# Kernel tuning notes

Hardware: AMD Instinct MI355X
Metric: run time of the kernel (lower is better)

Reference implementation:

```python
import jax, jax.numpy as jnp
import numpy as np

B = 2048          # batch
F = 32            # input feature size
H = 512           # lstm hidden size
BN = 64           # autoencoder bottleneck
OUT = 8           # final dense output size
SEQ_LEN = 128
LOOK_AHEAD = 32
RS, RE = 0, 8     # replace_start, replace_end (RE-RS == OUT)


def setup_inputs() -> dict:
    key = jax.random.key(0)
    ks = jax.random.split(key, 16)
    s = lambda k, shape: (jax.random.normal(k, shape, jnp.float32) * 0.05)
    return {
        'x': jax.random.normal(ks[0], (B, SEQ_LEN + LOOK_AHEAD, F), jnp.float32),
        # layer-0 LSTMCell (input F)
        'Wih0': s(ks[1], (F, 4 * H)), 'Whh0': s(ks[2], (H, 4 * H)),
        'bih0': s(ks[3], (4 * H,)),   'bhh0': s(ks[4], (4 * H,)),
        # layer-1 LSTMCell (input H)
        'Wih1': s(ks[5], (H, 4 * H)), 'Whh1': s(ks[6], (H, 4 * H)),
        'bih1': s(ks[7], (4 * H,)),   'bhh1': s(ks[8], (4 * H,)),
        # discretizing autoencoder: 2H -> BN -> 2H (shared across layers)
        'We': s(ks[9], (2 * H, BN)),  'be': s(ks[10], (BN,)),
        'Wd': s(ks[11], (BN, 2 * H)), 'bd': s(ks[12], (2 * H,)),
        # final dense H -> OUT
        'Wf': s(ks[13], (H, OUT)),    'bf': s(ks[14], (OUT,)),
    }


def _lstm_cell(x, h, c, Wih, Whh, bih, bhh):
    # torch.nn.LSTMCell gate order: i, f, g, o
    g = x @ Wih + bih + h @ Whh + bhh          # [B, 4H]
    i, f, gg, o = jnp.split(g, 4, axis=1)
    i, f, o = jax.nn.sigmoid(i), jax.nn.sigmoid(f), jax.nn.sigmoid(o)
    c2 = f * c + i * jnp.tanh(gg)
    return o * jnp.tanh(c2), c2


def _ae(z, We, be, Wd, bd):
    # bottleneck with straight-through rounding (discretization)
    b = jnp.tanh(z @ We + be)
    q = b + jax.lax.stop_gradient(jnp.round(b) - b)
    return q @ Wd + bd


def _layers_fwd(x_t, st, p):
    h0, c0, h1, c1 = st
    hc = _ae(jnp.concatenate([h0, c0], axis=1), p['We'], p['be'], p['Wd'], p['bd'])
    h0, c0 = jnp.split(hc, 2, axis=1)
    h0, c0 = _lstm_cell(x_t, h0, c0, p['Wih0'], p['Whh0'], p['bih0'], p['bhh0'])
    # dropout layer between stacked layers is identity in eval mode
    hc = _ae(jnp.concatenate([h1, c1], axis=1), p['We'], p['be'], p['Wd'], p['bd'])
    h1, c1 = jnp.split(hc, 2, axis=1)
    h1, c1 = _lstm_cell(h0, h1, c1, p['Wih1'], p['Whh1'], p['bih1'], p['bhh1'])
    return (h0, c0, h1, c1)


def reference(x, Wih0, Whh0, bih0, bhh0, Wih1, Whh1, bih1, bhh1,
              We, be, Wd, bd, Wf, bf):
    p = dict(Wih0=Wih0, Whh0=Whh0, bih0=bih0, bhh0=bhh0,
             Wih1=Wih1, Whh1=Whh1, bih1=bih1, bhh1=bhh1,
             We=We, be=be, Wd=Wd, bd=bd)
    bsz = x.shape[0]
    z = jnp.zeros((bsz, H), x.dtype)
    st = (z, z, z, z)

    # warm-up phase over seq_len observed steps
    def step1(st, x_t):
        return _layers_fwd(x_t, st, p), None
    st, _ = jax.lax.scan(step1, st, jnp.swapaxes(x[:, :SEQ_LEN], 0, 1))
    out0 = st[2] @ Wf + bf  # final dense on top-layer h

    def step2(carry, x_t):
        st, out = carry
        x_t = x_t.at[:, RS:RE].set(out)
        st = _layers_fwd(x_t, st, p)
        out = st[2] @ Wf + bf
        return (st, out), out
    (_, _), outs = jax.lax.scan(step2, (st, out0),
                                jnp.swapaxes(x[:, SEQ_LEN:SEQ_LEN + LOOK_AHEAD], 0, 1))

    # [B, 1 + look_ahead, OUT]
    return jnp.concatenate([out0[:, None, :], jnp.swapaxes(outs, 0, 1)], axis=1)
```

## Files before the change

kernel.cpp:

```cpp
#include <hip/hip_runtime.h>
#include <hip/hip_bf16.h>
#include <math.h>

#define NB    2048
#define FIN   32
#define HH    512
#define G4    2048
#define BNE   64
#define OUTD  8
#define SEQL  128
#define LOOK  32
#define TOT   (SEQL + LOOK)
#define TB    8
#define NTHR  1024

__device__ __forceinline__ float sigf(float v) { return 1.0f / (1.0f + expf(-v)); }

#define MAC2(S, HS)                                    \
  {                                                    \
    a[S].x = fmaf(w.x, (HS), a[S].x);                  \
    a[S].y = fmaf(w.y, (HS), a[S].y);                  \
  }
#define MAC2x8()                                       \
  {                                                    \
    MAC2(0, hA.x); MAC2(1, hA.y); MAC2(2, hA.z); MAC2(3, hA.w); \
    MAC2(4, hB.x); MAC2(5, hB.y); MAC2(6, hB.z); MAC2(7, hB.w); \
  }

__global__ __launch_bounds__(NTHR)
void fused_rnn(const float* __restrict__ x,
               const float* __restrict__ Wih0, const float* __restrict__ Whh0,
               const float* __restrict__ bih0, const float* __restrict__ bhh0,
               const float* __restrict__ Wih1, const float* __restrict__ Whh1,
               const float* __restrict__ bih1, const float* __restrict__ bhh1,
               const float* __restrict__ We,   const float* __restrict__ be,
               const float* __restrict__ Wd,   const float* __restrict__ bd,
               const float* __restrict__ Wf,   const float* __restrict__ bf,
               float* __restrict__ out)
{
  __shared__ float sh0[HH][TB], sc0[HH][TB], sh1[HH][TB], sc1[HH][TB];
  __shared__ float sg[TB][G4];
  __shared__ float sq[2][BNE][TB];
  __shared__ float sx[FIN][TB];
  __shared__ float sout[TB][OUTD];

  const int t  = threadIdx.x;
  const int b0 = blockIdx.x * TB;

  for (int i = t; i < HH * TB; i += NTHR) {
    (&sh0[0][0])[i] = 0.f; (&sc0[0][0])[i] = 0.f;
    (&sh1[0][0])[i] = 0.f; (&sc1[0][0])[i] = 0.f;
  }

  const float2 bb0 = make_float2(bih0[2*t]   + bhh0[2*t],
                                 bih0[2*t+1] + bhh0[2*t+1]);
  const float2 bb1 = make_float2(bih1[2*t]   + bhh1[2*t],
                                 bih1[2*t+1] + bhh1[2*t+1]);

  const double Athr = 0.5493061443340549;

  for (int step = 0; step < TOT; ++step) {
    __syncthreads();

    {
      const int ae = t >> 9, s = (t >> 6) & 7, n = t & 63;
      const float* Sh = ae ? &sh1[0][0] : &sh0[0][0];
      const float* Sc = ae ? &sc1[0][0] : &sc0[0][0];
      double a0 = (double)be[n];
      const float* we0 = We + n;
#pragma unroll 4
      for (int k = 0; k < HH; k++)
        a0 = fma((double)Sh[k * TB + s], (double)we0[(size_t)k * BNE], a0);
      const float* we1 = We + (size_t)HH * BNE + n;
#pragma unroll 4
      for (int k = 0; k < HH; k++)
        a0 = fma((double)Sc[k * TB + s], (double)we1[(size_t)k * BNE], a0);
      sq[ae][n][s] = (a0 > Athr) ? 1.f : ((a0 < -Athr) ? -1.f : 0.f);
    }
    __syncthreads();

    {
      float aq0[TB], aq1[TB];
      const float bdv = bd[t];
#pragma unroll
      for (int s = 0; s < TB; s++) { aq0[s] = bdv; aq1[s] = bdv; }
      const float* wd = Wd + t;
#pragma unroll 2
      for (int j = 0; j < BNE; j++) {
        const float w = wd[(size_t)j * (2 * HH)];
        const float4 qA0 = *(const float4*)&sq[0][j][0];
        const float4 qB0 = *(const float4*)&sq[0][j][4];
        const float4 qA1 = *(const float4*)&sq[1][j][0];
        const float4 qB1 = *(const float4*)&sq[1][j][4];
        aq0[0] = fmaf(qA0.x, w, aq0[0]); aq0[1] = fmaf(qA0.y, w, aq0[1]);
        aq0[2] = fmaf(qA0.z, w, aq0[2]); aq0[3] = fmaf(qA0.w, w, aq0[3]);
        aq0[4] = fmaf(qB0.x, w, aq0[4]); aq0[5] = fmaf(qB0.y, w, aq0[5]);
        aq0[6] = fmaf(qB0.z, w, aq0[6]); aq0[7] = fmaf(qB0.w, w, aq0[7]);
        aq1[0] = fmaf(qA1.x, w, aq1[0]); aq1[1] = fmaf(qA1.y, w, aq1[1]);
        aq1[2] = fmaf(qA1.z, w, aq1[2]); aq1[3] = fmaf(qA1.w, w, aq1[3]);
        aq1[4] = fmaf(qB1.x, w, aq1[4]); aq1[5] = fmaf(qB1.y, w, aq1[5]);
        aq1[6] = fmaf(qB1.z, w, aq1[6]); aq1[7] = fmaf(qB1.w, w, aq1[7]);
      }
      if (t < HH) {
#pragma unroll
        for (int s = 0; s < TB; s++) { sh0[t][s] = aq0[s]; sh1[t][s] = aq1[s]; }
      } else {
        const int c = t - HH;
#pragma unroll
        for (int s = 0; s < TB; s++) { sc0[c][s] = aq0[s]; sc1[c][s] = aq1[s]; }
      }
      if (t < FIN * TB) {
        int s = t >> 5, f = t & 31;
        float xv;
        if (step >= SEQL && f < OUTD) xv = sout[s][f];
        else xv = x[((size_t)(b0 + s) * TOT + step) * FIN + f];
        sx[f][s] = xv;
      }
    }
    __syncthreads();

    {
      float2 a[TB];
#pragma unroll
      for (int s = 0; s < TB; s++) a[s] = bb0;
      const float2* wx = (const float2*)Wih0 + t;
#pragma unroll 4
      for (int k = 0; k < FIN; k++) {
        const float2 w  = wx[(size_t)k * (G4 / 2)];
        const float4 hA = *(const float4*)&sx[k][0];
        const float4 hB = *(const float4*)&sx[k][4];
        MAC2x8();
      }
      const float2* wh = (const float2*)Whh0 + t;
#pragma unroll 8
      for (int k = 0; k < HH; k++) {
        const float2 w  = wh[(size_t)k * (G4 / 2)];
        const float4 hA = *(const float4*)&sh0[k][0];
        const float4 hB = *(const float4*)&sh0[k][4];
        MAC2x8();
      }
#pragma unroll
      for (int s = 0; s < TB; s++) *(float2*)&sg[s][2 * t] = a[s];
    }
    __syncthreads();
    {
      const int h  = t & (HH - 1);
      const int sb = (t >> 9) * 4;
#pragma unroll
      for (int s2 = 0; s2 < 4; s2++) {
        const int s = sb + s2;
        const float ig = sigf(sg[s][h]);
        const float fg = sigf(sg[s][HH + h]);
        const float gt = tanhf(sg[s][2 * HH + h]);
        const float og = sigf(sg[s][3 * HH + h]);
        const float c2 = fmaf(fg, sc0[h][s], ig * gt);
        sc0[h][s] = c2;
        sh0[h][s] = og * tanhf(c2);
      }
    }
    __syncthreads();

    {
      float2 a[TB];
#pragma unroll
      for (int s = 0; s < TB; s++) a[s] = bb1;
      const float2* wx = (const float2*)Wih1 + t;
#pragma unroll 8
      for (int k = 0; k < HH; k++) {
        const float2 w  = wx[(size_t)k * (G4 / 2)];
        const float4 hA = *(const float4*)&sh0[k][0];
        const float4 hB = *(const float4*)&sh0[k][4];
        MAC2x8();
      }
      const float2* wh = (const float2*)Whh1 + t;
#pragma unroll 8
      for (int k = 0; k < HH; k++) {
        const float2 w  = wh[(size_t)k * (G4 / 2)];
        const float4 hA = *(const float4*)&sh1[k][0];
        const float4 hB = *(const float4*)&sh1[k][4];
        MAC2x8();
      }
#pragma unroll
      for (int s = 0; s < TB; s++) *(float2*)&sg[s][2 * t] = a[s];
    }
    __syncthreads();
    {
      const int h  = t & (HH - 1);
      const int sb = (t >> 9) * 4;
#pragma unroll
      for (int s2 = 0; s2 < 4; s2++) {
        const int s = sb + s2;
        const float ig = sigf(sg[s][h]);
        const float fg = sigf(sg[s][HH + h]);
        const float gt = tanhf(sg[s][2 * HH + h]);
        const float og = sigf(sg[s][3 * HH + h]);
        const float c2 = fmaf(fg, sc1[h][s], ig * gt);
        sc1[h][s] = c2;
        sh1[h][s] = og * tanhf(c2);
      }
    }

    if (step >= SEQL - 1) {
      __syncthreads();
      if (t < TB * OUTD) {
        int s = t >> 3, o = t & 7;
        float a = bf[o];
#pragma unroll 4
        for (int k = 0; k < HH; k++) a = fmaf(sh1[k][s], Wf[k * OUTD + o], a);
        sout[s][o] = a;
        int slot = step - (SEQL - 1);
        out[((size_t)(b0 + s) * (1 + LOOK) + slot) * OUTD + o] = a;
      }
    }
  }
}

extern "C" void kernel_launch(void* const* d_in, const int* in_sizes, int n_in,
                              void* d_out, int out_size, void* d_ws, size_t ws_size,
                              hipStream_t stream) {
  const float* x    = (const float*)d_in[0];
  const float* Wih0 = (const float*)d_in[1];
  const float* Whh0 = (const float*)d_in[2];
  const float* bih0 = (const float*)d_in[3];
  const float* bhh0 = (const float*)d_in[4];
  const float* Wih1 = (const float*)d_in[5];
  const float* Whh1 = (const float*)d_in[6];
  const float* bih1 = (const float*)d_in[7];
  const float* bhh1 = (const float*)d_in[8];
  const float* We   = (const float*)d_in[9];
  const float* be   = (const float*)d_in[10];
  const float* Wd   = (const float*)d_in[11];
  const float* bd   = (const float*)d_in[12];
  const float* Wf   = (const float*)d_in[13];
  const float* bf   = (const float*)d_in[14];

  fused_rnn<<<NB / TB, NTHR, 0, stream>>>(x, Wih0, Whh0, bih0, bhh0,
                                          Wih1, Whh1, bih1, bhh1,
                                          We, be, Wd, bd, Wf, bf,
                                          (float*)d_out);
}
```

Measured before the change: 81.12 ms.

## Split each batch group's hidden units across four workgroups with global barriers

```diff
diff --git a/kernel.cpp b/kernel.cpp
--- a/kernel.cpp
+++ b/kernel.cpp
@@ -1,8 +1,6 @@
 #include <hip/hip_runtime.h>
-#include <hip/hip_bf16.h>
 #include <math.h>
 
-#define NB    2048
 #define FIN   32
 #define HH    512
 #define G4    2048
@@ -11,21 +9,39 @@
 #define SEQL  128
 #define LOOK  32
 #define TOT   (SEQL + LOOK)
-#define TB    8
+#define GS    32
 #define NTHR  1024
+#define NWG   256
+
+#define ST_SZ   (64 * HH * GS)
+#define WS_ST   1024
+#define WS_H0D  (WS_ST + 4 * ST_SZ)
+#define WS_H1D  (WS_H0D + ST_SZ)
+#define WS_TR   (WS_H1D + ST_SZ)
+#define WS_SOUT (WS_TR + 64 * 2 * BNE * GS)
 
 __device__ __forceinline__ float sigf(float v) { return 1.0f / (1.0f + expf(-v)); }
 
-#define MAC2(S, HS)                                    \
-  {                                                    \
-    a[S].x = fmaf(w.x, (HS), a[S].x);                  \
-    a[S].y = fmaf(w.y, (HS), a[S].y);                  \
+__device__ __forceinline__ void gbar(int* cnt, int target) {
+  __syncthreads();
+  if (threadIdx.x == 0) {
+    __hip_atomic_fetch_add(cnt, 1, __ATOMIC_ACQ_REL, __HIP_MEMORY_SCOPE_AGENT);
+    while (__hip_atomic_load(cnt, __ATOMIC_ACQUIRE, __HIP_MEMORY_SCOPE_AGENT) < target)
+      __builtin_amdgcn_s_sleep(4);
   }
-#define MAC2x8()                                       \
-  {                                                    \
-    MAC2(0, hA.x); MAC2(1, hA.y); MAC2(2, hA.z); MAC2(3, hA.w); \
-    MAC2(4, hB.x); MAC2(5, hB.y); MAC2(6, hB.z); MAC2(7, hB.w); \
-  }
+  __syncthreads();
+  __threadfence();
+}
+
+#define MACQ(HA, HB)                                            \
+  { a[0].x = fmaf(w.x, HA.x, a[0].x); a[0].y = fmaf(w.y, HA.x, a[0].y); \
+    a[1].x = fmaf(w.x, HA.y, a[1].x); a[1].y = fmaf(w.y, HA.y, a[1].y); \
+    a[2].x = fmaf(w.x, HA.z, a[2].x); a[2].y = fmaf(w.y, HA.z, a[2].y); \
+    a[3].x = fmaf(w.x, HA.w, a[3].x); a[3].y = fmaf(w.y, HA.w, a[3].y); \
+    a[4].x = fmaf(w.x, HB.x, a[4].x); a[4].y = fmaf(w.y, HB.x, a[4].y); \
+    a[5].x = fmaf(w.x, HB.y, a[5].x); a[5].y = fmaf(w.y, HB.y, a[5].y); \
+    a[6].x = fmaf(w.x, HB.z, a[6].x); a[6].y = fmaf(w.y, HB.z, a[6].y); \
+    a[7].x = fmaf(w.x, HB.w, a[7].x); a[7].y = fmaf(w.y, HB.w, a[7].y); }
 
 __global__ __launch_bounds__(NTHR)
 void fused_rnn(const float* __restrict__ x,
@@ -36,180 +52,200 @@
                const float* __restrict__ We,   const float* __restrict__ be,
                const float* __restrict__ Wd,   const float* __restrict__ bd,
                const float* __restrict__ Wf,   const float* __restrict__ bf,
-               float* __restrict__ out)
+               float* __restrict__ out, float* __restrict__ ws)
 {
-  __shared__ float sh0[HH][TB], sc0[HH][TB], sh1[HH][TB], sc1[HH][TB];
-  __shared__ float sg[TB][G4];
-  __shared__ float sq[2][BNE][TB];
-  __shared__ float sx[FIN][TB];
-  __shared__ float sout[TB][OUTD];
-
-  const int t  = threadIdx.x;
-  const int b0 = blockIdx.x * TB;
-
-  for (int i = t; i < HH * TB; i += NTHR) {
-    (&sh0[0][0])[i] = 0.f; (&sc0[0][0])[i] = 0.f;
-    (&sh1[0][0])[i] = 0.f; (&sc1[0][0])[i] = 0.f;
-  }
-
-  const float2 bb0 = make_float2(bih0[2*t]   + bhh0[2*t],
-                                 bih0[2*t+1] + bhh0[2*t+1]);
-  const float2 bb1 = make_float2(bih1[2*t]   + bhh1[2*t],
-                                 bih1[2*t+1] + bhh1[2*t+1]);
+  __shared__ float gbuf[GS][HH];
+  __shared__ float tq[2][BNE][GS];
+  __shared__ float cd[2][128][GS + 1];
+
+  const int t   = threadIdx.x;
+  const int bid = blockIdx.x;
+  const int G   = bid & 63;
+  const int Q   = bid >> 6;
+  const int S0  = G * GS;
+  const int UQ  = Q * 128;
+
+  int*   cnt = (int*)ws + G * 16;
+  float* h0c = ws + WS_ST + 0 * ST_SZ + G * (HH * GS);
+  float* c0c = ws + WS_ST + 1 * ST_SZ + G * (HH * GS);
+  float* h1c = ws + WS_ST + 2 * ST_SZ + G * (HH * GS);
+  float* c1c = ws + WS_ST + 3 * ST_SZ + G * (HH * GS);
+  float* h0d = ws + WS_H0D + G * (HH * GS);
+  float* h1d = ws + WS_H1D + G * (HH * GS);
+  float* trg = ws + WS_TR  + G * (2 * BNE * GS);
+  float* sog = ws + WS_SOUT + G * (GS * OUTD);
+
+  const int u = t & 255, v = t >> 8;
+  const int p = u >> 6, wl = u & 63;
+  const int cg = p * HH + UQ + 2 * wl;
+  const float2 bb0 = make_float2(bih0[cg] + bhh0[cg], bih0[cg + 1] + bhh0[cg + 1]);
+  const float2 bb1 = make_float2(bih1[cg] + bhh1[cg], bih1[cg + 1] + bhh1[cg + 1]);
+
+  const int cl = t & 255, sg2 = t >> 8;
+  const int dcol = (cl < 128) ? (UQ + cl) : (HH + UQ + (cl - 128));
+  const float bdv = bd[dcol];
+
+  const int ae = t >> 9, se = (t >> 6) & 7, n = t & 63;
+  const int sE = 8 * Q + se;
+
+  const int ul = t & 127, sq8 = t >> 7;
 
   const double Athr = 0.5493061443340549;
 
+  int bar = 0;
+
   for (int step = 0; step < TOT; ++step) {
-    __syncthreads();
-
-    {
-      const int ae = t >> 9, s = (t >> 6) & 7, n = t & 63;
-      const float* Sh = ae ? &sh1[0][0] : &sh0[0][0];
-      const float* Sc = ae ? &sc1[0][0] : &sc0[0][0];
+    {
+      const float* Sh = ae ? h1c : h0c;
+      const float* Sc = ae ? c1c : c0c;
       double a0 = (double)be[n];
-      const float* we0 = We + n;
+      const float* weh = We + n;
 #pragma unroll 4
       for (int k = 0; k < HH; k++)
-        a0 = fma((double)Sh[k * TB + s], (double)we0[(size_t)k * BNE], a0);
-      const float* we1 = We + (size_t)HH * BNE + n;
+        a0 = fma((double)Sh[k * GS + sE], (double)weh[(size_t)k * BNE], a0);
+      const float* wec = We + (size_t)HH * BNE + n;
 #pragma unroll 4
       for (int k = 0; k < HH; k++)
-        a0 = fma((double)Sc[k * TB + s], (double)we1[(size_t)k * BNE], a0);
-      sq[ae][n][s] = (a0 > Athr) ? 1.f : ((a0 < -Athr) ? -1.f : 0.f);
-    }
-    __syncthreads();
-
-    {
-      float aq0[TB], aq1[TB];
-      const float bdv = bd[t];
-#pragma unroll
-      for (int s = 0; s < TB; s++) { aq0[s] = bdv; aq1[s] = bdv; }
-      const float* wd = Wd + t;
+        a0 = fma((double)Sc[k * GS + sE], (double)wec[(size_t)k * BNE], a0);
+      trg[ae * (BNE * GS) + n * GS + sE] =
+          (a0 > Athr) ? 1.f : ((a0 < -Athr) ? -1.f : 0.f);
+    }
+    gbar(cnt, 4 * (++bar));
+
+    {
+      for (int i = t; i < 2 * BNE * GS; i += NTHR) (&tq[0][0][0])[i] = trg[i];
+      __syncthreads();
+      float ac0[8], ac1[8];
+#pragma unroll
+      for (int s = 0; s < 8; s++) { ac0[s] = bdv; ac1[s] = bdv; }
+      const float* wd = Wd + dcol;
 #pragma unroll 2
       for (int j = 0; j < BNE; j++) {
-        const float w = wd[(size_t)j * (2 * HH)];
-        const float4 qA0 = *(const float4*)&sq[0][j][0];
-        const float4 qB0 = *(const float4*)&sq[0][j][4];
-        const float4 qA1 = *(const float4*)&sq[1][j][0];
-        const float4 qB1 = *(const float4*)&sq[1][j][4];
-        aq0[0] = fmaf(qA0.x, w, aq0[0]); aq0[1] = fmaf(qA0.y, w, aq0[1]);
-        aq0[2] = fmaf(qA0.z, w, aq0[2]); aq0[3] = fmaf(qA0.w, w, aq0[3]);
-        aq0[4] = fmaf(qB0.x, w, aq0[4]); aq0[5] = fmaf(qB0.y, w, aq0[5]);
-        aq0[6] = fmaf(qB0.z, w, aq0[6]); aq0[7] = fmaf(qB0.w, w, aq0[7]);
-        aq1[0] = fmaf(qA1.x, w, aq1[0]); aq1[1] = fmaf(qA1.y, w, aq1[1]);
-        aq1[2] = fmaf(qA1.z, w, aq1[2]); aq1[3] = fmaf(qA1.w, w, aq1[3]);
-        aq1[4] = fmaf(qB1.x, w, aq1[4]); aq1[5] = fmaf(qB1.y, w, aq1[5]);
-        aq1[6] = fmaf(qB1.z, w, aq1[6]); aq1[7] = fmaf(qB1.w, w, aq1[7]);
-      }
-      if (t < HH) {
-#pragma unroll
-        for (int s = 0; s < TB; s++) { sh0[t][s] = aq0[s]; sh1[t][s] = aq1[s]; }
+        const float wv = wd[(size_t)j * (2 * HH)];
+        const float4 qA0 = *(const float4*)&tq[0][j][8 * sg2];
+        const float4 qB0 = *(const float4*)&tq[0][j][8 * sg2 + 4];
+        const float4 qA1 = *(const float4*)&tq[1][j][8 * sg2];
+        const float4 qB1 = *(const float4*)&tq[1][j][8 * sg2 + 4];
+        ac0[0] = fmaf(qA0.x, wv, ac0[0]); ac0[1] = fmaf(qA0.y, wv, ac0[1]);
+        ac0[2] = fmaf(qA0.z, wv, ac0[2]); ac0[3] = fmaf(qA0.w, wv, ac0[3]);
+        ac0[4] = fmaf(qB0.x, wv, ac0[4]); ac0[5] = fmaf(qB0.y, wv, ac0[5]);
+        ac0[6] = fmaf(qB0.z, wv, ac0[6]); ac0[7] = fmaf(qB0.w, wv, ac0[7]);
+        ac1[0] = fmaf(qA1.x, wv, ac1[0]); ac1[1] = fmaf(qA1.y, wv, ac1[1]);
+        ac1[2] = fmaf(qA1.z, wv, ac1[2]); ac1[3] = fmaf(qA1.w, wv, ac1[3]);
+        ac1[4] = fmaf(qB1.x, wv, ac1[4]); ac1[5] = fmaf(qB1.y, wv, ac1[5]);
+        ac1[6] = fmaf(qB1.z, wv, ac1[6]); ac1[7] = fmaf(qB1.w, wv, ac1[7]);
+      }
+      if (cl < 128) {
+        const int row = (UQ + cl) * GS + 8 * sg2;
+#pragma unroll
+        for (int s = 0; s < 8; s++) { h0d[row + s] = ac0[s]; h1d[row + s] = ac1[s]; }
       } else {
-        const int c = t - HH;
-#pragma unroll
-        for (int s = 0; s < TB; s++) { sc0[c][s] = aq0[s]; sc1[c][s] = aq1[s]; }
-      }
-      if (t < FIN * TB) {
-        int s = t >> 5, f = t & 31;
+#pragma unroll
+        for (int s = 0; s < 8; s++) {
+          cd[0][cl - 128][8 * sg2 + s] = ac0[s];
+          cd[1][cl - 128][8 * sg2 + s] = ac1[s];
+        }
+      }
+    }
+    gbar(cnt, 4 * (++bar));
+
+    {
+      float* sxT = &tq[0][0][0];
+      { int s = t >> 5, f = t & 31;
         float xv;
-        if (step >= SEQL && f < OUTD) xv = sout[s][f];
-        else xv = x[((size_t)(b0 + s) * TOT + step) * FIN + f];
-        sx[f][s] = xv;
-      }
-    }
-    __syncthreads();
-
-    {
-      float2 a[TB];
-#pragma unroll
-      for (int s = 0; s < TB; s++) a[s] = bb0;
-      const float2* wx = (const float2*)Wih0 + t;
+        if (step >= SEQL && f < OUTD) xv = sog[s * OUTD + f];
+        else xv = x[((size_t)(S0 + s) * TOT + step) * FIN + f];
+        sxT[f * GS + s] = xv; }
+      __syncthreads();
+
+      float2 a[8];
+#pragma unroll
+      for (int s = 0; s < 8; s++) a[s] = bb0;
+      const float2* wx = (const float2*)(Wih0 + cg);
 #pragma unroll 4
       for (int k = 0; k < FIN; k++) {
         const float2 w  = wx[(size_t)k * (G4 / 2)];
-        const float4 hA = *(const float4*)&sx[k][0];
-        const float4 hB = *(const float4*)&sx[k][4];
-        MAC2x8();
-      }
-      const float2* wh = (const float2*)Whh0 + t;
+        const float4 hA = *(const float4*)&sxT[k * GS + 8 * v];
+        const float4 hB = *(const float4*)&sxT[k * GS + 8 * v + 4];
+        MACQ(hA, hB);
+      }
+      const float2* wh = (const float2*)(Whh0 + cg);
 #pragma unroll 8
       for (int k = 0; k < HH; k++) {
         const float2 w  = wh[(size_t)k * (G4 / 2)];
-        const float4 hA = *(const float4*)&sh0[k][0];
-        const float4 hB = *(const float4*)&sh0[k][4];
-        MAC2x8();
-      }
-#pragma unroll
-      for (int s = 0; s < TB; s++) *(float2*)&sg[s][2 * t] = a[s];
-    }
-    __syncthreads();
-    {
-      const int h  = t & (HH - 1);
-      const int sb = (t >> 9) * 4;
-#pragma unroll
-      for (int s2 = 0; s2 < 4; s2++) {
-        const int s = sb + s2;
-        const float ig = sigf(sg[s][h]);
-        const float fg = sigf(sg[s][HH + h]);
-        const float gt = tanhf(sg[s][2 * HH + h]);
-        const float og = sigf(sg[s][3 * HH + h]);
-        const float c2 = fmaf(fg, sc0[h][s], ig * gt);
-        sc0[h][s] = c2;
-        sh0[h][s] = og * tanhf(c2);
-      }
-    }
-    __syncthreads();
-
-    {
-      float2 a[TB];
-#pragma unroll
-      for (int s = 0; s < TB; s++) a[s] = bb1;
-      const float2* wx = (const float2*)Wih1 + t;
+        const float4 hA = *(const float4*)&h0d[k * GS + 8 * v];
+        const float4 hB = *(const float4*)&h0d[k * GS + 8 * v + 4];
+        MACQ(hA, hB);
+      }
+      __syncthreads();
+#pragma unroll
+      for (int s = 0; s < 8; s++)
+        *(float2*)&gbuf[8 * v + s][p * 128 + 2 * wl] = a[s];
+      __syncthreads();
+#pragma unroll
+      for (int i = 0; i < 4; i++) {
+        const int s = sq8 * 4 + i;
+        const float ig = sigf(gbuf[s][ul]);
+        const float fg = sigf(gbuf[s][128 + ul]);
+        const float gt = tanhf(gbuf[s][256 + ul]);
+        const float og = sigf(gbuf[s][384 + ul]);
+        const float c2 = fmaf(fg, cd[0][ul][s], ig * gt);
+        h0c[(UQ + ul) * GS + s] = og * tanhf(c2);
+        c0c[(UQ + ul) * GS + s] = c2;
+      }
+    }
+    gbar(cnt, 4 * (++bar));
+
+    {
+      float2 a[8];
+#pragma unroll
+      for (int s = 0; s < 8; s++) a[s] = bb1;
+      const float2* wx = (const float2*)(Wih1 + cg);
 #pragma unroll 8
       for (int k = 0; k < HH; k++) {
         const float2 w  = wx[(size_t)k * (G4 / 2)];
-        const float4 hA = *(const float4*)&sh0[k][0];
-        const float4 hB = *(const float4*)&sh0[k][4];
-        MAC2x8();
-      }
-      const float2* wh = (const float2*)Whh1 + t;
+        const float4 hA = *(const float4*)&h0c[k * GS + 8 * v];
+        const float4 hB = *(const float4*)&h0c[k * GS + 8 * v + 4];
+        MACQ(hA, hB);
+      }
+      const float2* wh = (const float2*)(Whh1 + cg);
 #pragma unroll 8
       for (int k = 0; k < HH; k++) {
         const float2 w  = wh[(size_t)k * (G4 / 2)];
-        const float4 hA = *(const float4*)&sh1[k][0];
-        const float4 hB = *(const float4*)&sh1[k][4];
-        MAC2x8();
-      }
-#pragma unroll
-      for (int s = 0; s < TB; s++) *(float2*)&sg[s][2 * t] = a[s];
-    }
-    __syncthreads();
-    {
-      const int h  = t & (HH - 1);
-      const int sb = (t >> 9) * 4;
-#pragma unroll
-      for (int s2 = 0; s2 < 4; s2++) {
-        const int s = sb + s2;
-        const float ig = sigf(sg[s][h]);
-        const float fg = sigf(sg[s][HH + h]);
-        const float gt = tanhf(sg[s][2 * HH + h]);
-        const float og = sigf(sg[s][3 * HH + h]);
-        const float c2 = fmaf(fg, sc1[h][s], ig * gt);
-        sc1[h][s] = c2;
-        sh1[h][s] = og * tanhf(c2);
-      }
-    }
+        const float4 hA = *(const float4*)&h1d[k * GS + 8 * v];
+        const float4 hB = *(const float4*)&h1d[k * GS + 8 * v + 4];
+        MACQ(hA, hB);
+      }
+      __syncthreads();
+#pragma unroll
+      for (int s = 0; s < 8; s++)
+        *(float2*)&gbuf[8 * v + s][p * 128 + 2 * wl] = a[s];
+      __syncthreads();
+#pragma unroll
+      for (int i = 0; i < 4; i++) {
+        const int s = sq8 * 4 + i;
+        const float ig = sigf(gbuf[s][ul]);
+        const float fg = sigf(gbuf[s][128 + ul]);
+        const float gt = tanhf(gbuf[s][256 + ul]);
+        const float og = sigf(gbuf[s][384 + ul]);
+        const float c2 = fmaf(fg, cd[1][ul][s], ig * gt);
+        h1c[(UQ + ul) * GS + s] = og * tanhf(c2);
+        c1c[(UQ + ul) * GS + s] = c2;
+      }
+    }
+    gbar(cnt, 4 * (++bar));
 
     if (step >= SEQL - 1) {
-      __syncthreads();
-      if (t < TB * OUTD) {
-        int s = t >> 3, o = t & 7;
-        float a = bf[o];
-#pragma unroll 4
-        for (int k = 0; k < HH; k++) a = fmaf(sh1[k][s], Wf[k * OUTD + o], a);
-        sout[s][o] = a;
-        int slot = step - (SEQL - 1);
-        out[((size_t)(b0 + s) * (1 + LOOK) + slot) * OUTD + o] = a;
+      if (t < 8 * OUTD) {
+        const int s8 = t >> 3, o = t & 7;
+        const int sl = 8 * Q + s8;
+        float acc = bf[o];
+#pragma unroll 4
+        for (int k = 0; k < HH; k++)
+          acc = fmaf(h1c[k * GS + sl], Wf[k * OUTD + o], acc);
+        sog[sl * OUTD + o] = acc;
+        const int slot = step - (SEQL - 1);
+        out[((size_t)(S0 + sl) * (1 + LOOK) + slot) * OUTD + o] = acc;
       }
     }
   }
@@ -234,8 +270,10 @@
   const float* Wf   = (const float*)d_in[13];
   const float* bf   = (const float*)d_in[14];
 
-  fused_rnn<<<NB / TB, NTHR, 0, stream>>>(x, Wih0, Whh0, bih0, bhh0,
-                                          Wih1, Whh1, bih1, bhh1,
-                                          We, be, Wd, bd, Wf, bf,
-                                          (float*)d_out);
+  hipMemsetAsync(d_ws, 0, (size_t)(WS_ST + 4 * ST_SZ) * sizeof(float), stream);
+
+  fused_rnn<<<NWG, NTHR, 0, stream>>>(x, Wih0, Whh0, bih0, bhh0,
+                                      Wih1, Whh1, bih1, bhh1,
+                                      We, be, Wd, bd, Wf, bf,
+                                      (float*)d_out, (float*)d_ws);
 }
```

After: 206.8 ms. 2.55x slower.

## Fuse LSTM gate activations into gate GEMV with 512-thread gate-aligned mapping

Applied to the files above, without the earlier changes.

```diff
diff --git a/kernel.cpp b/kernel.cpp
--- a/kernel.cpp
+++ b/kernel.cpp
@@ -1,5 +1,4 @@
 #include <hip/hip_runtime.h>
-#include <hip/hip_bf16.h>
 #include <math.h>
 
 #define NB    2048
@@ -12,20 +11,15 @@
 #define LOOK  32
 #define TOT   (SEQL + LOOK)
 #define TB    8
-#define NTHR  1024
+#define NTHR  512
 
 __device__ __forceinline__ float sigf(float v) { return 1.0f / (1.0f + expf(-v)); }
 
-#define MAC2(S, HS)                                    \
-  {                                                    \
-    a[S].x = fmaf(w.x, (HS), a[S].x);                  \
-    a[S].y = fmaf(w.y, (HS), a[S].y);                  \
-  }
-#define MAC2x8()                                       \
-  {                                                    \
-    MAC2(0, hA.x); MAC2(1, hA.y); MAC2(2, hA.z); MAC2(3, hA.w); \
-    MAC2(4, hB.x); MAC2(5, hB.y); MAC2(6, hB.z); MAC2(7, hB.w); \
-  }
+#define GMAC4(A, W)                                                     \
+  { A[0].x = fmaf((W).x, hv.x, A[0].x); A[0].y = fmaf((W).y, hv.x, A[0].y); \
+    A[1].x = fmaf((W).x, hv.y, A[1].x); A[1].y = fmaf((W).y, hv.y, A[1].y); \
+    A[2].x = fmaf((W).x, hv.z, A[2].x); A[2].y = fmaf((W).y, hv.z, A[2].y); \
+    A[3].x = fmaf((W).x, hv.w, A[3].x); A[3].y = fmaf((W).y, hv.w, A[3].y); }
 
 __global__ __launch_bounds__(NTHR)
 void fused_rnn(const float* __restrict__ x,
@@ -39,8 +33,7 @@
                float* __restrict__ out)
 {
   __shared__ float sh0[HH][TB], sc0[HH][TB], sh1[HH][TB], sc1[HH][TB];
-  __shared__ float sg[TB][G4];
-  __shared__ float sq[2][BNE][TB];
+  __shared__ float tq[2][BNE][TB];
   __shared__ float sx[FIN][TB];
   __shared__ float sout[TB][OUTD];
 
@@ -52,10 +45,21 @@
     (&sh1[0][0])[i] = 0.f; (&sc1[0][0])[i] = 0.f;
   }
 
-  const float2 bb0 = make_float2(bih0[2*t]   + bhh0[2*t],
-                                 bih0[2*t+1] + bhh0[2*t+1]);
-  const float2 bb1 = make_float2(bih1[2*t]   + bhh1[2*t],
-                                 bih1[2*t+1] + bhh1[2*t+1]);
+  const int q  = t & 255;
+  const int sh = t >> 8;
+  const int s4 = 4 * sh;
+  const int u0 = 2 * q;
+  float2 bg0[4], bg1[4];
+#pragma unroll
+  for (int m = 0; m < 4; m++) {
+    const int c = m * HH + u0;
+    bg0[m] = make_float2(bih0[c] + bhh0[c], bih0[c + 1] + bhh0[c + 1]);
+    bg1[m] = make_float2(bih1[c] + bhh1[c], bih1[c + 1] + bhh1[c + 1]);
+  }
+
+  const int ae = t >> 8, n = t & 63, sp = (t >> 6) & 3;
+
+  const float bdx = bd[2 * t], bdy = bd[2 * t + 1];
 
   const double Athr = 0.5493061443340549;
 
@@ -63,51 +67,79 @@
     __syncthreads();
 
     {
-      const int ae = t >> 9, s = (t >> 6) & 7, n = t & 63;
       const float* Sh = ae ? &sh1[0][0] : &sh0[0][0];
       const float* Sc = ae ? &sc1[0][0] : &sc0[0][0];
-      double a0 = (double)be[n];
-      const float* we0 = We + n;
-#pragma unroll 4
-      for (int k = 0; k < HH; k++)
-        a0 = fma((double)Sh[k * TB + s], (double)we0[(size_t)k * BNE], a0);
-      const float* we1 = We + (size_t)HH * BNE + n;
-#pragma unroll 4
-      for (int k = 0; k < HH; k++)
-        a0 = fma((double)Sc[k * TB + s], (double)we1[(size_t)k * BNE], a0);
-      sq[ae][n][s] = (a0 > Athr) ? 1.f : ((a0 < -Athr) ? -1.f : 0.f);
-    }
-    __syncthreads();
-
-    {
-      float aq0[TB], aq1[TB];
-      const float bdv = bd[t];
-#pragma unroll
-      for (int s = 0; s < TB; s++) { aq0[s] = bdv; aq1[s] = bdv; }
-      const float* wd = Wd + t;
+      double a0 = (double)be[n], a1 = a0;
+      const float* weh = We + n;
+#pragma unroll 4
+      for (int k = 0; k < HH; k++) {
+        const float2 zz = *(const float2*)&Sh[k * TB + 2 * sp];
+        const double wv = (double)weh[(size_t)k * BNE];
+        a0 = fma((double)zz.x, wv, a0);
+        a1 = fma((double)zz.y, wv, a1);
+      }
+      const float* wec = We + (size_t)HH * BNE + n;
+#pragma unroll 4
+      for (int k = 0; k < HH; k++) {
+        const float2 zz = *(const float2*)&Sc[k * TB + 2 * sp];
+        const double wv = (double)wec[(size_t)k * BNE];
+        a0 = fma((double)zz.x, wv, a0);
+        a1 = fma((double)zz.y, wv, a1);
+      }
+      tq[ae][n][2 * sp]     = (a0 > Athr) ? 1.f : ((a0 < -Athr) ? -1.f : 0.f);
+      tq[ae][n][2 * sp + 1] = (a1 > Athr) ? 1.f : ((a1 < -Athr) ? -1.f : 0.f);
+    }
+    __syncthreads();
+
+    {
+      float2 d0[TB], d1[TB];
+#pragma unroll
+      for (int s = 0; s < TB; s++) { d0[s] = make_float2(bdx, bdy); d1[s] = d0[s]; }
+      const float* wd = Wd + 2 * t;
 #pragma unroll 2
       for (int j = 0; j < BNE; j++) {
-        const float w = wd[(size_t)j * (2 * HH)];
-        const float4 qA0 = *(const float4*)&sq[0][j][0];
-        const float4 qB0 = *(const float4*)&sq[0][j][4];
-        const float4 qA1 = *(const float4*)&sq[1][j][0];
-        const float4 qB1 = *(const float4*)&sq[1][j][4];
-        aq0[0] = fmaf(qA0.x, w, aq0[0]); aq0[1] = fmaf(qA0.y, w, aq0[1]);
-        aq0[2] = fmaf(qA0.z, w, aq0[2]); aq0[3] = fmaf(qA0.w, w, aq0[3]);
-        aq0[4] = fmaf(qB0.x, w, aq0[4]); aq0[5] = fmaf(qB0.y, w, aq0[5]);
-        aq0[6] = fmaf(qB0.z, w, aq0[6]); aq0[7] = fmaf(qB0.w, w, aq0[7]);
-        aq1[0] = fmaf(qA1.x, w, aq1[0]); aq1[1] = fmaf(qA1.y, w, aq1[1]);
-        aq1[2] = fmaf(qA1.z, w, aq1[2]); aq1[3] = fmaf(qA1.w, w, aq1[3]);
-        aq1[4] = fmaf(qB1.x, w, aq1[4]); aq1[5] = fmaf(qB1.y, w, aq1[5]);
-        aq1[6] = fmaf(qB1.z, w, aq1[6]); aq1[7] = fmaf(qB1.w, w, aq1[7]);
-      }
-      if (t < HH) {
-#pragma unroll
-        for (int s = 0; s < TB; s++) { sh0[t][s] = aq0[s]; sh1[t][s] = aq1[s]; }
+        const float2 w = *(const float2*)&wd[(size_t)j * (2 * HH)];
+        const float4 qA0 = *(const float4*)&tq[0][j][0];
+        const float4 qB0 = *(const float4*)&tq[0][j][4];
+        const float4 qA1 = *(const float4*)&tq[1][j][0];
+        const float4 qB1 = *(const float4*)&tq[1][j][4];
+        d0[0].x = fmaf(qA0.x, w.x, d0[0].x); d0[0].y = fmaf(qA0.x, w.y, d0[0].y);
+        d0[1].x = fmaf(qA0.y, w.x, d0[1].x); d0[1].y = fmaf(qA0.y, w.y, d0[1].y);
+        d0[2].x = fmaf(qA0.z, w.x, d0[2].x); d0[2].y = fmaf(qA0.z, w.y, d0[2].y);
+        d0[3].x = fmaf(qA0.w, w.x, d0[3].x); d0[3].y = fmaf(qA0.w, w.y, d0[3].y);
+        d0[4].x = fmaf(qB0.x, w.x, d0[4].x); d0[4].y = fmaf(qB0.x, w.y, d0[4].y);
+        d0[5].x = fmaf(qB0.y, w.x, d0[5].x); d0[5].y = fmaf(qB0.y, w.y, d0[5].y);
+        d0[6].x = fmaf(qB0.z, w.x, d0[6].x); d0[6].y = fmaf(qB0.z, w.y, d0[6].y);
+        d0[7].x = fmaf(qB0.w, w.x, d0[7].x); d0[7].y = fmaf(qB0.w, w.y, d0[7].y);
+        d1[0].x = fmaf(qA1.x, w.x, d1[0].x); d1[0].y = fmaf(qA1.x, w.y, d1[0].y);
+        d1[1].x = fmaf(qA1.y, w.x, d1[1].x); d1[1].y = fmaf(qA1.y, w.y, d1[1].y);
+        d1[2].x = fmaf(qA1.z, w.x, d1[2].x); d1[2].y = fmaf(qA1.z, w.y, d1[2].y);
+        d1[3].x = fmaf(qA1.w, w.x, d1[3].x); d1[3].y = fmaf(qA1.w, w.y, d1[3].y);
+        d1[4].x = fmaf(qB1.x, w.x, d1[4].x); d1[4].y = fmaf(qB1.x, w.y, d1[4].y);
+        d1[5].x = fmaf(qB1.y, w.x, d1[5].x); d1[5].y = fmaf(qB1.y, w.y, d1[5].y);
+        d1[6].x = fmaf(qB1.z, w.x, d1[6].x); d1[6].y = fmaf(qB1.z, w.y, d1[6].y);
+        d1[7].x = fmaf(qB1.w, w.x, d1[7].x); d1[7].y = fmaf(qB1.w, w.y, d1[7].y);
+      }
+      if (t < 256) {
+        const int u = 2 * t;
+        *(float4*)&sh0[u][0]     = make_float4(d0[0].x, d0[1].x, d0[2].x, d0[3].x);
+        *(float4*)&sh0[u][4]     = make_float4(d0[4].x, d0[5].x, d0[6].x, d0[7].x);
+        *(float4*)&sh0[u + 1][0] = make_float4(d0[0].y, d0[1].y, d0[2].y, d0[3].y);
+        *(float4*)&sh0[u + 1][4] = make_float4(d0[4].y, d0[5].y, d0[6].y, d0[7].y);
+        *(float4*)&sh1[u][0]     = make_float4(d1[0].x, d1[1].x, d1[2].x, d1[3].x);
+        *(float4*)&sh1[u][4]     = make_float4(d1[4].x, d1[5].x, d1[6].x, d1[7].x);
+        *(float4*)&sh1[u + 1][0] = make_float4(d1[0].y, d1[1].y, d1[2].y, d1[3].y);
+        *(float4*)&sh1[u + 1][4] = make_float4(d1[4].y, d1[5].y, d1[6].y, d1[7].y);
       } else {
-        const int c = t - HH;
-#pragma unroll
-        for (int s = 0; s < TB; s++) { sc0[c][s] = aq0[s]; sc1[c][s] = aq1[s]; }
+        const int u = 2 * t - HH;
+        *(float4*)&sc0[u][0]     = make_float4(d0[0].x, d0[1].x, d0[2].x, d0[3].x);
+        *(float4*)&sc0[u][4]     = make_float4(d0[4].x, d0[5].x, d0[6].x, d0[7].x);
+        *(float4*)&sc0[u + 1][0] = make_float4(d0[0].y, d0[1].y, d0[2].y, d0[3].y);
+        *(float4*)&sc0[u + 1][4] = make_float4(d0[4].y, d0[5].y, d0[6].y, d0[7].y);
+        *(float4*)&sc1[u][0]     = make_float4(d1[0].x, d1[1].x, d1[2].x, d1[3].x);
+        *(float4*)&sc1[u][4]     = make_float4(d1[4].x, d1[5].x, d1[6].x, d1[7].x);
+        *(float4*)&sc1[u + 1][0] = make_float4(d1[0].y, d1[1].y, d1[2].y, d1[3].y);
+        *(float4*)&sc1[u + 1][4] = make_float4(d1[4].y, d1[5].y, d1[6].y, d1[7].y);
       }
       if (t < FIN * TB) {
         int s = t >> 5, f = t & 31;
@@ -120,84 +152,110 @@
     __syncthreads();
 
     {
-      float2 a[TB];
-#pragma unroll
-      for (int s = 0; s < TB; s++) a[s] = bb0;
-      const float2* wx = (const float2*)Wih0 + t;
-#pragma unroll 4
-      for (int k = 0; k < FIN; k++) {
-        const float2 w  = wx[(size_t)k * (G4 / 2)];
-        const float4 hA = *(const float4*)&sx[k][0];
-        const float4 hB = *(const float4*)&sx[k][4];
-        MAC2x8();
-      }
-      const float2* wh = (const float2*)Whh0 + t;
+      float2 gI[4], gF[4], gG[4], gO[4];
+#pragma unroll
+      for (int i = 0; i < 4; i++) { gI[i] = bg0[0]; gF[i] = bg0[1]; gG[i] = bg0[2]; gO[i] = bg0[3]; }
+      {
+        const float* row = Wih0 + u0;
+#pragma unroll 4
+        for (int k = 0; k < FIN; k++, row += G4) {
+          const float2 wI = *(const float2*)(row);
+          const float2 wF = *(const float2*)(row + HH);
+          const float2 wG = *(const float2*)(row + 2 * HH);
+          const float2 wO = *(const float2*)(row + 3 * HH);
+          const float4 hv = *(const float4*)&sx[k][s4];
+          GMAC4(gI, wI); GMAC4(gF, wF); GMAC4(gG, wG); GMAC4(gO, wO);
+        }
+      }
+      {
+        const float* row = Whh0 + u0;
 #pragma unroll 8
-      for (int k = 0; k < HH; k++) {
-        const float2 w  = wh[(size_t)k * (G4 / 2)];
-        const float4 hA = *(const float4*)&sh0[k][0];
-        const float4 hB = *(const float4*)&sh0[k][4];
-        MAC2x8();
-      }
-#pragma unroll
-      for (int s = 0; s < TB; s++) *(float2*)&sg[s][2 * t] = a[s];
-    }
-    __syncthreads();
-    {
-      const int h  = t & (HH - 1);
-      const int sb = (t >> 9) * 4;
-#pragma unroll
-      for (int s2 = 0; s2 < 4; s2++) {
-        const int s = sb + s2;
-        const float ig = sigf(sg[s][h]);
-        const float fg = sigf(sg[s][HH + h]);
-        const float gt = tanhf(sg[s][2 * HH + h]);
-        const float og = sigf(sg[s][3 * HH + h]);
-        const float c2 = fmaf(fg, sc0[h][s], ig * gt);
-        sc0[h][s] = c2;
-        sh0[h][s] = og * tanhf(c2);
-      }
-    }
-    __syncthreads();
-
-    {
-      float2 a[TB];
-#pragma unroll
-      for (int s = 0; s < TB; s++) a[s] = bb1;
-      const float2* wx = (const float2*)Wih1 + t;
+        for (int k = 0; k < HH; k++, row += G4) {
+          const float2 wI = *(const float2*)(row);
+          const float2 wF = *(const float2*)(row + HH);
+          const float2 wG = *(const float2*)(row + 2 * HH);
+          const float2 wO = *(const float2*)(row + 3 * HH);
+          const float4 hv = *(const float4*)&sh0[k][s4];
+          GMAC4(gI, wI); GMAC4(gF, wF); GMAC4(gG, wG); GMAC4(gO, wO);
+        }
+      }
+      const float4 cA = *(const float4*)&sc0[u0][s4];
+      const float4 cB = *(const float4*)&sc0[u0 + 1][s4];
+      const float coldA[4] = { cA.x, cA.y, cA.z, cA.w };
+      const float coldB[4] = { cB.x, cB.y, cB.z, cB.w };
+      float4 hnA, hnB, cnA, cnB;
+      float* hA = (float*)&hnA; float* hB = (float*)&hnB;
+      float* cnAp = (float*)&cnA; float* cnBp = (float*)&cnB;
+#pragma unroll
+      for (int i = 0; i < 4; i++) {
+        float ig = sigf(gI[i].x), fg = sigf(gF[i].x);
+        float gt = tanhf(gG[i].x), og = sigf(gO[i].x);
+        float c2 = fmaf(fg, coldA[i], ig * gt);
+        cnAp[i] = c2; hA[i] = og * tanhf(c2);
+        ig = sigf(gI[i].y); fg = sigf(gF[i].y);
+        gt = tanhf(gG[i].y); og = sigf(gO[i].y);
+        c2 = fmaf(fg, coldB[i], ig * gt);
+        cnBp[i] = c2; hB[i] = og * tanhf(c2);
+      }
+      __syncthreads();
+      *(float4*)&sh0[u0][s4]     = hnA;
+      *(float4*)&sh0[u0 + 1][s4] = hnB;
+      *(float4*)&sc0[u0][s4]     = cnA;
+      *(float4*)&sc0[u0 + 1][s4] = cnB;
+    }
+    __syncthreads();
+
+    {
+      float2 gI[4], gF[4], gG[4], gO[4];
+#pragma unroll
+      for (int i = 0; i < 4; i++) { gI[i] = bg1[0]; gF[i] = bg1[1]; gG[i] = bg1[2]; gO[i] = bg1[3]; }
+      {
+        const float* row = Wih1 + u0;
 #pragma unroll 8
-      for (int k = 0; k < HH; k++) {
-        const float2 w  = wx[(size_t)k * (G4 / 2)];
-        const float4 hA = *(const float4*)&sh0[k][0];
-        const float4 hB = *(const float4*)&sh0[k][4];
-        MAC2x8();
-      }
-      const float2* wh = (const float2*)Whh1 + t;
+        for (int k = 0; k < HH; k++, row += G4) {
+          const float2 wI = *(const float2*)(row);
+          const float2 wF = *(const float2*)(row + HH);
+          const float2 wG = *(const float2*)(row + 2 * HH);
+          const float2 wO = *(const float2*)(row + 3 * HH);
+          const float4 hv = *(const float4*)&sh0[k][s4];
+          GMAC4(gI, wI); GMAC4(gF, wF); GMAC4(gG, wG); GMAC4(gO, wO);
+        }
+      }
+      {
+        const float* row = Whh1 + u0;
 #pragma unroll 8
-      for (int k = 0; k < HH; k++) {
-        const float2 w  = wh[(size_t)k * (G4 / 2)];
-        const float4 hA = *(const float4*)&sh1[k][0];
-        const float4 hB = *(const float4*)&sh1[k][4];
-        MAC2x8();
-      }
-#pragma unroll
-      for (int s = 0; s < TB; s++) *(float2*)&sg[s][2 * t] = a[s];
-    }
-    __syncthreads();
-    {
-      const int h  = t & (HH - 1);
-      const int sb = (t >> 9) * 4;
-#pragma unroll
-      for (int s2 = 0; s2 < 4; s2++) {
-        const int s = sb + s2;
-        const float ig = sigf(sg[s][h]);
-        const float fg = sigf(sg[s][HH + h]);
-        const float gt = tanhf(sg[s][2 * HH + h]);
-        const float og = sigf(sg[s][3 * HH + h]);
-        const float c2 = fmaf(fg, sc1[h][s], ig * gt);
-        sc1[h][s] = c2;
-        sh1[h][s] = og * tanhf(c2);
-      }
+        for (int k = 0; k < HH; k++, row += G4) {
+          const float2 wI = *(const float2*)(row);
+          const float2 wF = *(const float2*)(row + HH);
+          const float2 wG = *(const float2*)(row + 2 * HH);
+          const float2 wO = *(const float2*)(row + 3 * HH);
+          const float4 hv = *(const float4*)&sh1[k][s4];
+          GMAC4(gI, wI); GMAC4(gF, wF); GMAC4(gG, wG); GMAC4(gO, wO);
+        }
+      }
+      const float4 cA = *(const float4*)&sc1[u0][s4];
+      const float4 cB = *(const float4*)&sc1[u0 + 1][s4];
+      const float coldA[4] = { cA.x, cA.y, cA.z, cA.w };
+      const float coldB[4] = { cB.x, cB.y, cB.z, cB.w };
+      float4 hnA, hnB, cnA, cnB;
+      float* hA = (float*)&hnA; float* hB = (float*)&hnB;
+      float* cnAp = (float*)&cnA; float* cnBp = (float*)&cnB;
+#pragma unroll
+      for (int i = 0; i < 4; i++) {
+        float ig = sigf(gI[i].x), fg = sigf(gF[i].x);
+        float gt = tanhf(gG[i].x), og = sigf(gO[i].x);
+        float c2 = fmaf(fg, coldA[i], ig * gt);
+        cnAp[i] = c2; hA[i] = og * tanhf(c2);
+        ig = sigf(gI[i].y); fg = sigf(gF[i].y);
+        gt = tanhf(gG[i].y); og = sigf(gO[i].y);
+        c2 = fmaf(fg, coldB[i], ig * gt);
+        cnBp[i] = c2; hB[i] = og * tanhf(c2);
+      }
+      __syncthreads();
+      *(float4*)&sh1[u0][s4]     = hnA;
+      *(float4*)&sh1[u0 + 1][s4] = hnB;
+      *(float4*)&sc1[u0][s4]     = cnA;
+      *(float4*)&sc1[u0 + 1][s4] = cnB;
     }
 
     if (step >= SEQL - 1) {
```

Result: slower. 92.00 ms (+13.4%).
